# Performance work log

Measured on AMD Instinct MI355X. Metric: run time of the kernel, lower is better.

## Reference

```python
import jax, jax.numpy as jnp
import numpy as np

ALPHA = 0.2  # LeakyReLU negative slope


def setup_inputs() -> dict:
    key = jax.random.key(0)
    k1, k2, k3, k4, k5 = jax.random.split(key, 5)
    n, fin, fout = 4096, 512, 512
    X = jax.random.normal(k1, (n, fin), dtype=jnp.float32)
    # sparse-ish 0/1 adjacency with self loops so every softmax row is non-empty
    A = (jax.random.uniform(k2, (n, n)) < 0.005).astype(jnp.float32)
    A = jnp.minimum(A + jnp.eye(n, dtype=jnp.float32), 1.0)
    W_short = jax.random.normal(k3, (fout, fin), dtype=jnp.float32) * 0.02
    r = jax.random.normal(k4, (2 * fout, 1), dtype=jnp.float32) * 0.02
    W_long = jax.random.normal(k5, (fout, fin), dtype=jnp.float32) * 0.02
    return dict(X=X, A=A, W_short=W_short, r=r, W_long=W_long, num_hops=3)


def reference(X, A, W_short, r, W_long, num_hops):
    fout = W_short.shape[0]
    neg_inf = jnp.finfo(X.dtype).min

    # ---- ShortDistanceAttention ----
    Wh = X @ W_short.T                                   # (n, fout)
    # r^T [Wh_i || Wh_j] = (Wh_i . r_src) + (Wh_j . r_dst)
    src = Wh @ r[:fout, 0]                               # (n,)
    dst = Wh @ r[fout:, 0]                               # (n,)
    e = jax.nn.leaky_relu(src[:, None] + dst[None, :], ALPHA)  # (n, n)
    edge_mask = A != 0
    att = jax.nn.softmax(jnp.where(edge_mask, e, neg_inf), axis=1)
    hk = jax.nn.gelu(att @ Wh)                           # (n, fout)

    # ---- LongDistanceAttention ----
    Wa = X @ W_long.T                                    # (n, fout)
    # multi-hop reachability: union of nonzero patterns of A^1..A^num_hops
    Ak = A
    reach = A
    for _ in range(num_hops - 1):
        Ak = Ak @ A                                      # dense n^3 matmul
        reach = reach + Ak
    hop_mask = reach != 0
    scores = hk @ Wa.T                                   # (n, n)
    att2 = jax.nn.softmax(jnp.where(hop_mask, scores, neg_inf), axis=1)
    ok = att2 @ hk                                       # (n, fout)
    return ok
```

## Files before the change

### kernel.cpp

```cpp
#include <hip/hip_runtime.h>
#include <math.h>


#define N_NODES 4096
#define FDIM    512
#define MAX_NNZ 128
#define LRELU_ALPHA 0.2f
#define NUM_HOPS 3
#define PSCALE 9.765625e-4f

typedef unsigned short ushort_t;
typedef unsigned long long u64;
typedef __attribute__((ext_vector_type(8))) __bf16 bf16x8;
typedef __attribute__((ext_vector_type(8))) _Float16 f16x8;
typedef __attribute__((ext_vector_type(2))) _Float16 f16x2;
typedef __attribute__((ext_vector_type(4))) float f32x4;
typedef __attribute__((ext_vector_type(16))) float f32x16;

__device__ __forceinline__ ushort_t f2bf(float x) {
    unsigned u = __float_as_uint(x);
    u += 0x7fff + ((u >> 16) & 1);
    return (ushort_t)(u >> 16);
}
__device__ __forceinline__ float bf2f(ushort_t h) {
    return __uint_as_float((unsigned)h << 16);
}
__device__ __forceinline__ void split2(float x, ushort_t& h, ushort_t& l) {
    h = f2bf(x);
    l = f2bf(x - bf2f(h));
}
__device__ __forceinline__ ushort_t f2h(float x) {
    _Float16 v = (_Float16)x;
    return *(ushort_t*)&v;
}

__device__ __forceinline__ float gelu_tanh(float x) {
    float x3 = x * x * x;
    float t  = tanhf(0.7978845608028654f * (x + 0.044715f * x3));
    return 0.5f * x * (1.0f + t);
}

__device__ __forceinline__ void gload_lds16(const void* g, void* l) {
    __builtin_amdgcn_global_load_lds(
        (const __attribute__((address_space(1))) unsigned int*)g,
        (__attribute__((address_space(3))) unsigned int*)l, 16, 0, 0);
}

__global__ __launch_bounds__(256) void split_all(const float4* __restrict__ X,
                                                 const float4* __restrict__ Ws,
                                                 const float4* __restrict__ Wl,
                                                 ushort4* __restrict__ Xh,
                                                 ushort4* __restrict__ Xl,
                                                 ushort4* __restrict__ Wch,
                                                 ushort4* __restrict__ Wcl) {
    const int n0 = N_NODES * FDIM / 4;
    const int n1 = FDIM * FDIM / 4;
    const int total = n0 + 2 * n1;
    int i = blockIdx.x * 256 + threadIdx.x;
    int stride = gridDim.x * 256;
    for (; i < total; i += stride) {
        float4 v;
        ushort4* dh;
        ushort4* dl;
        int o;
        if (i < n0)           { v = X[i];  dh = Xh;       dl = Xl;       o = i; }
        else if (i < n0 + n1) { o = i - n0;      v = Ws[o]; dh = Wch;      dl = Wcl; }
        else                  { o = i - n0 - n1; v = Wl[o]; dh = Wch + n1; dl = Wcl + n1; }
        ushort4 h, l;
        split2(v.x, h.x, l.x); split2(v.y, h.y, l.y);
        split2(v.z, h.z, l.z); split2(v.w, h.w, l.w);
        dh[o] = h; dl[o] = l;
    }
}

__global__ __launch_bounds__(256) void transpose_f16(const ushort_t* __restrict__ src,
                                                     ushort_t* __restrict__ tf) {
    __shared__ ushort_t tile[32][33];
    int bx = blockIdx.x;
    int by = blockIdx.y;
    int tx = threadIdx.x & 31;
    int ty = threadIdx.x >> 5;
    for (int r = ty; r < 32; r += 8)
        tile[r][tx] = src[(size_t)(by * 32 + r) * FDIM + bx * 32 + tx];
    __syncthreads();
    for (int r = ty; r < 32; r += 8)
        tf[(size_t)(bx * 32 + r) * N_NODES + by * 32 + tx] = tile[tx][r];
}

__global__ __launch_bounds__(256) void gemm_score(
    const ushort_t* __restrict__ Af, int lda,
    const ushort_t* __restrict__ Bf, int ldb,
    ushort_t* __restrict__ Pout, int ldc,
    const u64* __restrict__ mask, int K) {
    constexpr int BM = 128, BN = 128;
    constexpr int WTN = BN / 2, JT = WTN / 32;

    __shared__ ushort_t As[BM * 32];
    __shared__ ushort_t Bs[BN * 32];
    __shared__ u64 mw[BM][2];

    int t = threadIdx.x;
    int wave = t >> 6, lane = t & 63;
    int wr = wave >> 1, wc = wave & 1;
    int row0 = blockIdx.y * BM, col0 = blockIdx.x * BN;

    f32x16 acc[2][JT] = {};
    int m32 = lane & 31;
    int e   = lane >> 5;

    int rr = t >> 2;
    int cs = (t & 3) ^ ((t >> 3) & 3);
    const ushort_t* pA[BM / 64];
    const ushort_t* pB[BN / 64];
#pragma unroll
    for (int q = 0; q < BM / 64; q++)
        pA[q] = Af + (size_t)(row0 + q * 64 + rr) * lda + cs * 8;
#pragma unroll
    for (int q = 0; q < BN / 64; q++)
        pB[q] = Bf + (size_t)(col0 + q * 64 + rr) * ldb + cs * 8;

    for (int ks = 0; ks < K; ks += 32) {
#pragma unroll
        for (int q = 0; q < BM / 64; q++) {
            gload_lds16(pA[q], As + (q * 256 + wave * 64) * 8);
            pA[q] += 32;
        }
#pragma unroll
        for (int q = 0; q < BN / 64; q++) {
            gload_lds16(pB[q], Bs + (q * 256 + wave * 64) * 8);
            pB[q] += 32;
        }
        __syncthreads();

        f16x8 af[2][2], bf[JT][2];
#pragma unroll
        for (int i = 0; i < 2; i++) {
            int ar = wr * 64 + i * 32 + m32;
            int sw = (ar >> 1) & 3;
#pragma unroll
            for (int kh = 0; kh < 2; kh++) {
                int slot = (kh * 2 + e) ^ sw;
                af[i][kh] = *(const f16x8*)(As + ar * 32 + slot * 8);
            }
        }
#pragma unroll
        for (int j = 0; j < JT; j++) {
            int bc = wc * WTN + j * 32 + m32;
            int sw = (bc >> 1) & 3;
#pragma unroll
            for (int kh = 0; kh < 2; kh++) {
                int slot = (kh * 2 + e) ^ sw;
                bf[j][kh] = *(const f16x8*)(Bs + bc * 32 + slot * 8);
            }
        }
#pragma unroll
        for (int i = 0; i < 2; i++)
#pragma unroll
            for (int j = 0; j < JT; j++)
#pragma unroll
                for (int kh = 0; kh < 2; kh++)
                    acc[i][j] = __builtin_amdgcn_mfma_f32_32x32x16_f16(af[i][kh], bf[j][kh], acc[i][j], 0, 0, 0);
        __syncthreads();
    }

    if (t < 2 * BM) {
        int r2 = t >> 1, w2 = t & 1;
        mw[r2][w2] = mask[(size_t)(row0 + r2) * 64 + (col0 >> 6) + w2];
    }
    __syncthreads();

    int rbase = 4 * e;
#pragma unroll
    for (int i = 0; i < 2; i++)
#pragma unroll
        for (int j = 0; j < JT; j++) {
            int cl = wc * WTN + j * 32 + m32;
            int col = col0 + cl;
#pragma unroll
            for (int rg = 0; rg < 16; rg++) {
                int rl = wr * 64 + i * 32 + (rg & 3) + 8 * (rg >> 2) + rbase;
                bool on = (mw[rl][cl >> 6] >> (cl & 63)) & 1ULL;
                float pv = on ? __expf(acc[i][j][rg]) * PSCALE : 0.0f;
                Pout[(size_t)(row0 + rl) * ldc + col] = f2h(pv);
            }
        }
}

__global__ __launch_bounds__(256) void gemm_pv(
    const ushort_t* __restrict__ Pf, int lda,
    const ushort_t* __restrict__ Bf, int ldb,
    float* __restrict__ Cf, int ldc,
    float* __restrict__ lsum, int M, int Klen) {
    constexpr int BM = 128, BN = 64;
    constexpr int WTN = BN / 2, JT = WTN / 32;

    __shared__ ushort_t As[BM * 32];
    __shared__ ushort_t Bs[BN * 32];

    int bid = blockIdx.x;
    int r8 = bid & 7;
    int g  = bid >> 3;
    int bx = g & 7;
    int yz = (g >> 3) * 8 + r8;
    int by = yz & 31, bz = yz >> 5;

    int t = threadIdx.x;
    int wave = t >> 6, lane = t & 63;
    int wr = wave >> 1, wc = wave & 1;
    int row0 = by * BM, col0 = bx * BN;
    int kb = bz * Klen;
    Cf += (size_t)bz * M * ldc;

    f32x16 acc[2][JT] = {};
    float rs[2] = {0.0f, 0.0f};
    int m32 = lane & 31;
    int e   = lane >> 5;

    int rr = t >> 2;
    int cs = (t & 3) ^ ((t >> 3) & 3);
    const ushort_t* pA[BM / 64];
#pragma unroll
    for (int q = 0; q < BM / 64; q++)
        pA[q] = Pf + (size_t)(row0 + q * 64 + rr) * lda + kb + cs * 8;
    const ushort_t* pB = Bf + (size_t)(col0 + rr) * ldb + kb + cs * 8;

    for (int ks = 0; ks < Klen; ks += 32) {
#pragma unroll
        for (int q = 0; q < BM / 64; q++) {
            gload_lds16(pA[q], As + (q * 256 + wave * 64) * 8);
            pA[q] += 32;
        }
        if (wave < 1) {
        }
        gload_lds16(pB, Bs + (wave * 64) * 8);
        pB += 32;
        __syncthreads();

        f16x8 af[2][2], bf[JT][2];
#pragma unroll
        for (int i = 0; i < 2; i++) {
            int ar = wr * 64 + i * 32 + m32;
            int sw = (ar >> 1) & 3;
#pragma unroll
            for (int kh = 0; kh < 2; kh++) {
                int slot = (kh * 2 + e) ^ sw;
                f16x8 raw = *(const f16x8*)(As + ar * 32 + slot * 8);
                af[i][kh] = raw;
                if (wc == 0) {
#pragma unroll
                    for (int k = 0; k < 8; k++) rs[i] += (float)raw[k];
                }
            }
        }
#pragma unroll
        for (int j = 0; j < JT; j++) {
            int bc = wc * WTN + j * 32 + m32;
            int sw = (bc >> 1) & 3;
#pragma unroll
            for (int kh = 0; kh < 2; kh++) {
                int slot = (kh * 2 + e) ^ sw;
                bf[j][kh] = *(const f16x8*)(Bs + bc * 32 + slot * 8);
            }
        }
#pragma unroll
        for (int i = 0; i < 2; i++)
#pragma unroll
            for (int j = 0; j < JT; j++)
#pragma unroll
                for (int kh = 0; kh < 2; kh++)
                    acc[i][j] = __builtin_amdgcn_mfma_f32_32x32x16_f16(af[i][kh], bf[j][kh], acc[i][j], 0, 0, 0);
        __syncthreads();
    }

    if (wc == 0) {
        rs[0] += __shfl_xor(rs[0], 32, 64);
        rs[1] += __shfl_xor(rs[1], 32, 64);
        if (bx == 0 && e == 0) {
            atomicAdd(&lsum[row0 + wr * 64 + m32], rs[0]);
            atomicAdd(&lsum[row0 + wr * 64 + 32 + m32], rs[1]);
        }
    }

    int rbase = 4 * e;
#pragma unroll
    for (int i = 0; i < 2; i++)
#pragma unroll
        for (int j = 0; j < JT; j++) {
            int col = col0 + wc * WTN + j * 32 + m32;
#pragma unroll
            for (int rg = 0; rg < 16; rg++) {
                int row = row0 + wr * 64 + i * 32 + (rg & 3) + 8 * (rg >> 2) + rbase;
                Cf[(size_t)row * ldc + col] = acc[i][j][rg];
            }
        }
}

template <int BM, int BN>
__global__ __launch_bounds__(256) void gemm3_nt(
    const ushort_t* __restrict__ Ah, const ushort_t* __restrict__ Al, int lda,
    const ushort_t* __restrict__ Bh, const ushort_t* __restrict__ Bl, int ldb,
    float* __restrict__ Cf, int ldc, int Klen,
    ushort_t* __restrict__ Whf, ushort_t* __restrict__ Ef) {
    constexpr int WTN = BN / 2;
    constexpr int JT  = WTN / 32;

    __shared__ ushort_t As_h[BM * 32], As_l[BM * 32];
    __shared__ ushort_t Bs_h[BN * 32], Bs_l[BN * 32];

    int t = threadIdx.x;
    int wave = t >> 6, lane = t & 63;
    int wr = wave >> 1, wc = wave & 1;
    int row0 = blockIdx.y * BM, col0 = blockIdx.x * BN;

    f32x16 acc[2][JT] = {};
    int m32 = lane & 31;
    int e   = lane >> 5;

    int rr = t >> 2;
    int cs = (t & 3) ^ ((t >> 3) & 3);
    const ushort_t* pAh[BM / 64];
    const ushort_t* pAl[BM / 64];
    const ushort_t* pBh[BN / 64];
    const ushort_t* pBl[BN / 64];
#pragma unroll
    for (int q = 0; q < BM / 64; q++) {
        size_t o = (size_t)(row0 + q * 64 + rr) * lda + cs * 8;
        pAh[q] = Ah + o; pAl[q] = Al + o;
    }
#pragma unroll
    for (int q = 0; q < BN / 64; q++) {
        size_t o = (size_t)(col0 + q * 64 + rr) * ldb + cs * 8;
        pBh[q] = Bh + o; pBl[q] = Bl + o;
    }

    for (int ks = 0; ks < Klen; ks += 32) {
#pragma unroll
        for (int q = 0; q < BM / 64; q++) {
            int ldsoff = (q * 256 + wave * 64) * 8;
            gload_lds16(pAh[q], As_h + ldsoff);
            gload_lds16(pAl[q], As_l + ldsoff);
            pAh[q] += 32; pAl[q] += 32;
        }
#pragma unroll
        for (int q = 0; q < BN / 64; q++) {
            int ldsoff = (q * 256 + wave * 64) * 8;
            gload_lds16(pBh[q], Bs_h + ldsoff);
            gload_lds16(pBl[q], Bs_l + ldsoff);
            pBh[q] += 32; pBl[q] += 32;
        }
        __syncthreads();

        bf16x8 afh[2][2], afl[2][2], bfh[JT][2], bfl[JT][2];
#pragma unroll
        for (int i = 0; i < 2; i++) {
            int ar = wr * 64 + i * 32 + m32;
            int sw = (ar >> 1) & 3;
#pragma unroll
            for (int kh = 0; kh < 2; kh++) {
                int slot = (kh * 2 + e) ^ sw;
                afh[i][kh] = *(const bf16x8*)(As_h + ar * 32 + slot * 8);
                afl[i][kh] = *(const bf16x8*)(As_l + ar * 32 + slot * 8);
            }
        }
#pragma unroll
        for (int j = 0; j < JT; j++) {
            int bc = wc * WTN + j * 32 + m32;
            int sw = (bc >> 1) & 3;
#pragma unroll
            for (int kh = 0; kh < 2; kh++) {
                int slot = (kh * 2 + e) ^ sw;
                bfh[j][kh] = *(const bf16x8*)(Bs_h + bc * 32 + slot * 8);
                bfl[j][kh] = *(const bf16x8*)(Bs_l + bc * 32 + slot * 8);
            }
        }
#pragma unroll
        for (int i = 0; i < 2; i++)
#pragma unroll
            for (int j = 0; j < JT; j++)
#pragma unroll
                for (int kh = 0; kh < 2; kh++) {
                    acc[i][j] = __builtin_amdgcn_mfma_f32_32x32x16_bf16(afh[i][kh], bfh[j][kh], acc[i][j], 0, 0, 0);
                    acc[i][j] = __builtin_amdgcn_mfma_f32_32x32x16_bf16(afh[i][kh], bfl[j][kh], acc[i][j], 0, 0, 0);
                    acc[i][j] = __builtin_amdgcn_mfma_f32_32x32x16_bf16(afl[i][kh], bfh[j][kh], acc[i][j], 0, 0, 0);
                }
        __syncthreads();
    }

    int rbase = 4 * e;
#pragma unroll
    for (int i = 0; i < 2; i++)
#pragma unroll
        for (int j = 0; j < JT; j++) {
            int col = col0 + wc * WTN + j * 32 + m32;
#pragma unroll
            for (int rg = 0; rg < 16; rg++) {
                int row = row0 + wr * 64 + i * 32 + (rg & 3) + 8 * (rg >> 2) + rbase;
                float v = acc[i][j][rg];
                if (col < FDIM) {
                    Cf[(size_t)row * ldc + col] = v;
                    Whf[(size_t)row * FDIM + col] = f2h(v);
                } else {
                    Ef[(size_t)row * FDIM + col - FDIM] = f2h(v);
                }
            }
        }
}

__global__ __launch_bounds__(256) void reduce4(const f32x4* __restrict__ P,
                                               const float* __restrict__ lsum,
                                               f32x4* __restrict__ out) {
    const size_t stride = (size_t)N_NODES * FDIM / 4;
    int i = blockIdx.x * 256 + threadIdx.x;
    f32x4 s = P[i] + P[i + stride] + P[i + 2 * stride] + P[i + 3 * stride];
    float inv = 1.0f / lsum[i >> 7];
    out[i] = s * inv;
}

__global__ __launch_bounds__(256) void srcdst_kernel(const float* __restrict__ Wh,
                                                     const float* __restrict__ r,
                                                     float* __restrict__ src,
                                                     float* __restrict__ dst) {
    int i = blockIdx.x, t = threadIdx.x;
    float ps = 0.0f, pd = 0.0f;
    for (int k = t; k < FDIM; k += 256) {
        float w = Wh[(size_t)i * FDIM + k];
        ps += w * r[k];
        pd += w * r[FDIM + k];
    }
    __shared__ float sbuf[512];
    sbuf[t] = ps; sbuf[256 + t] = pd;
    __syncthreads();
    for (int s = 128; s > 0; s >>= 1) {
        if (t < s) { sbuf[t] += sbuf[t + s]; sbuf[256 + t] += sbuf[256 + t + s]; }
        __syncthreads();
    }
    if (t == 0) { src[i] = sbuf[0]; dst[i] = sbuf[256]; }
}

__global__ __launch_bounds__(256) void prep_A(const float* __restrict__ A,
                                              int* __restrict__ nnz,
                                              int* __restrict__ idx,
                                              u64* __restrict__ bits,
                                              u64* __restrict__ reach) {
    int i = blockIdx.x, t = threadIdx.x;
    int wave = t >> 6, lane = t & 63;
    __shared__ int cnt;
    if (t == 0) cnt = 0;
    __syncthreads();
    for (int w = wave; w < 64; w += 4) {
        float a = A[(size_t)i * N_NODES + w * 64 + lane];
        bool nz = a != 0.0f;
        u64 m = __ballot(nz);
        if (lane == 0) { bits[i * 64 + w] = m; reach[i * 64 + w] = m; }
        if (nz) {
            int s = atomicAdd(&cnt, 1);
            if (s < MAX_NNZ) idx[i * MAX_NNZ + s] = w * 64 + lane;
        }
    }
    __syncthreads();
    if (t == 0) nnz[i] = cnt < MAX_NNZ ? cnt : MAX_NNZ;
}

__global__ __launch_bounds__(256) void hop_kernel(const u64* __restrict__ in,
                                                  u64* __restrict__ out,
                                                  u64* __restrict__ reach,
                                                  const int* __restrict__ nnz,
                                                  const int* __restrict__ idx) {
    int i = blockIdx.x * 4 + (threadIdx.x >> 6);
    int w = threadIdx.x & 63;
    int cnt = nnz[i];
    u64 acc = 0ULL;
    for (int q = 0; q < cnt; q++) {
        int j = idx[i * MAX_NNZ + q];
        acc |= in[(size_t)j * 64 + w];
    }
    out[i * 64 + w] = acc;
    reach[i * 64 + w] |= acc;
}

__global__ __launch_bounds__(256) void short_attn(const ushort_t* __restrict__ Whf,
                                                  const float* __restrict__ src,
                                                  const float* __restrict__ dst,
                                                  const int* __restrict__ nnz,
                                                  const int* __restrict__ idx,
                                                  ushort_t* __restrict__ hkf) {
    int i = blockIdx.x, t = threadIdx.x;
    __shared__ int   s_idx[MAX_NNZ];
    __shared__ float s_w[MAX_NNZ];
    __shared__ float s_m, s_sum;
    int cnt = nnz[i];
    float si = src[i];
    if (t < cnt) {
        int j = idx[i * MAX_NNZ + t];
        s_idx[t] = j;
        float e = si + dst[j];
        s_w[t] = e > 0.0f ? e : LRELU_ALPHA * e;
    }
    __syncthreads();
    if (t == 0) {
        float m = -INFINITY;
        for (int q = 0; q < cnt; q++) m = fmaxf(m, s_w[q]);
        s_m = m;
    }
    __syncthreads();
    if (t < cnt) s_w[t] = __expf(s_w[t] - s_m);
    __syncthreads();
    if (t == 0) {
        float s = 0.0f;
        for (int q = 0; q < cnt; q++) s += s_w[q];
        s_sum = s;
    }
    __syncthreads();
    float inv = 1.0f / s_sum;
    const f16x2* W2 = (const f16x2*)Whf;
    float ax = 0.0f, ay = 0.0f;
    for (int q = 0; q < cnt; q++) {
        float w = s_w[q];
        f16x2 v = W2[(size_t)s_idx[q] * (FDIM / 2) + t];
        ax += w * (float)v.x; ay += w * (float)v.y;
    }
    float vx = gelu_tanh(ax * inv);
    float vy = gelu_tanh(ay * inv);
    size_t o = (size_t)i * FDIM + 2 * t;
    hkf[o] = f2h(vx); hkf[o + 1] = f2h(vy);
}

extern "C" void kernel_launch(void* const* d_in, const int* in_sizes, int n_in,
                              void* d_out, int out_size, void* d_ws, size_t ws_size,
                              hipStream_t stream) {
    (void)in_sizes; (void)n_in; (void)out_size; (void)ws_size;
    const float* X       = (const float*)d_in[0];
    const float* A       = (const float*)d_in[1];
    const float* W_short = (const float*)d_in[2];
    const float* r       = (const float*)d_in[3];
    const float* W_long  = (const float*)d_in[4];

    char* p = (char*)d_ws;
    ushort_t* scoresF = (ushort_t*)p; p += (size_t)N_NODES * N_NODES * 2;
    float* Psplit = (float*)p;   p += (size_t)4 * N_NODES * FDIM * 4;
    float* Wh     = (float*)p;   p += (size_t)N_NODES * FDIM * 4;
    ushort_t* Whf = (ushort_t*)p; p += (size_t)N_NODES * FDIM * 2;
    ushort_t* Xh  = (ushort_t*)p; p += (size_t)N_NODES * FDIM * 2;
    ushort_t* Xl  = (ushort_t*)p; p += (size_t)N_NODES * FDIM * 2;
    ushort_t* Waf = (ushort_t*)p; p += (size_t)N_NODES * FDIM * 2;
    ushort_t* Wch = (ushort_t*)p; p += (size_t)1024 * FDIM * 2;
    ushort_t* Wcl = (ushort_t*)p; p += (size_t)1024 * FDIM * 2;
    int* idx      = (int*)p;     p += (size_t)N_NODES * MAX_NNZ * 4;
    u64* Abits    = (u64*)p;     p += (size_t)N_NODES * 64 * 8;
    u64* Bcur     = (u64*)p;     p += (size_t)N_NODES * 64 * 8;
    u64* Bnxt     = (u64*)p;     p += (size_t)N_NODES * 64 * 8;
    u64* reach    = (u64*)p;     p += (size_t)N_NODES * 64 * 8;
    float* lsum   = (float*)p;   p += N_NODES * 4;
    float* src    = (float*)p;   p += N_NODES * 4;
    float* dst    = (float*)p;   p += N_NODES * 4;
    int* nnz      = (int*)p;     p += N_NODES * 4;

    ushort_t* hkf  = Xh;
    ushort_t* hkTf = (ushort_t*)Wh;

    hipMemsetAsync(lsum, 0, N_NODES * 4, stream);

    split_all<<<1280, 256, 0, stream>>>((const float4*)X, (const float4*)W_short,
                                        (const float4*)W_long,
                                        (ushort4*)Xh, (ushort4*)Xl,
                                        (ushort4*)Wch, (ushort4*)Wcl);

    gemm3_nt<128, 64><<<dim3(1024 / 64, N_NODES / 128), 256, 0, stream>>>(
        Xh, Xl, FDIM, Wch, Wcl, FDIM, Wh, FDIM, FDIM, Whf, Waf);

    srcdst_kernel<<<N_NODES, 256, 0, stream>>>(Wh, r, src, dst);

    prep_A<<<N_NODES, 256, 0, stream>>>(A, nnz, idx, Abits, reach);
    const u64* in_b = Abits;
    u64* out_b = Bcur;
    for (int h = 0; h < NUM_HOPS - 1; h++) {
        hop_kernel<<<N_NODES / 4, 256, 0, stream>>>(in_b, out_b, reach, nnz, idx);
        in_b = out_b;
        out_b = (out_b == Bcur) ? Bnxt : Bcur;
    }

    short_attn<<<N_NODES, 256, 0, stream>>>(Whf, src, dst, nnz, idx, hkf);

    transpose_f16<<<dim3(FDIM / 32, N_NODES / 32), 256, 0, stream>>>(hkf, hkTf);

    gemm_score<<<dim3(N_NODES / 128, N_NODES / 128), 256, 0, stream>>>(
        hkf, FDIM, Waf, FDIM, scoresF, N_NODES, reach, FDIM);

    gemm_pv<<<1024, 256, 0, stream>>>(
        scoresF, N_NODES, hkTf, N_NODES, Psplit, FDIM, lsum, N_NODES, N_NODES / 4);

    reduce4<<<2048, 256, 0, stream>>>((const f32x4*)Psplit, lsum, (f32x4*)d_out);
}
```

Measured before the change: 282.3 us.

## Halve gemm_score row tile and add grouped block swizzle

The score GEMM tile shrinks from 128x128 to 64x128. Each wave now holds one 32-row fragment instead of two, which doubles the grid to 2048 blocks. A 1D block index with an 8-row grouping swizzle replaces the 2D grid, meant to improve L2 reuse of the B operand across neighbouring blocks. The intent is better occupancy and load balance from fewer accumulators and more blocks, at the cost of lower arithmetic intensity per block. An empty leftover branch in gemm_pv is also removed.

```diff
diff --git a/kernel.cpp b/kernel.cpp
--- a/kernel.cpp
+++ b/kernel.cpp
@@ -92,39 +92,39 @@
     const ushort_t* __restrict__ Bf, int ldb,
     ushort_t* __restrict__ Pout, int ldc,
     const u64* __restrict__ mask, int K) {
-    constexpr int BM = 128, BN = 128;
+    constexpr int BM = 64, BN = 128;
     constexpr int WTN = BN / 2, JT = WTN / 32;
 
     __shared__ ushort_t As[BM * 32];
     __shared__ ushort_t Bs[BN * 32];
     __shared__ u64 mw[BM][2];
 
+    int bid = blockIdx.x;
+    int r8 = bid & 7;
+    int g  = bid >> 3;
+    int bxt = g & 31;
+    int byt = (g >> 5) * 8 + r8;
+
     int t = threadIdx.x;
     int wave = t >> 6, lane = t & 63;
     int wr = wave >> 1, wc = wave & 1;
-    int row0 = blockIdx.y * BM, col0 = blockIdx.x * BN;
-
-    f32x16 acc[2][JT] = {};
+    int row0 = byt * BM, col0 = bxt * BN;
+
+    f32x16 acc[JT] = {};
     int m32 = lane & 31;
     int e   = lane >> 5;
 
     int rr = t >> 2;
     int cs = (t & 3) ^ ((t >> 3) & 3);
-    const ushort_t* pA[BM / 64];
+    const ushort_t* pA = Af + (size_t)(row0 + rr) * lda + cs * 8;
     const ushort_t* pB[BN / 64];
-#pragma unroll
-    for (int q = 0; q < BM / 64; q++)
-        pA[q] = Af + (size_t)(row0 + q * 64 + rr) * lda + cs * 8;
 #pragma unroll
     for (int q = 0; q < BN / 64; q++)
         pB[q] = Bf + (size_t)(col0 + q * 64 + rr) * ldb + cs * 8;
 
     for (int ks = 0; ks < K; ks += 32) {
-#pragma unroll
-        for (int q = 0; q < BM / 64; q++) {
-            gload_lds16(pA[q], As + (q * 256 + wave * 64) * 8);
-            pA[q] += 32;
-        }
+        gload_lds16(pA, As + (wave * 64) * 8);
+        pA += 32;
 #pragma unroll
         for (int q = 0; q < BN / 64; q++) {
             gload_lds16(pB[q], Bs + (q * 256 + wave * 64) * 8);
@@ -132,15 +132,14 @@
         }
         __syncthreads();
 
-        f16x8 af[2][2], bf[JT][2];
-#pragma unroll
-        for (int i = 0; i < 2; i++) {
-            int ar = wr * 64 + i * 32 + m32;
+        f16x8 af[2], bf[JT][2];
+        {
+            int ar = wr * 32 + m32;
             int sw = (ar >> 1) & 3;
 #pragma unroll
             for (int kh = 0; kh < 2; kh++) {
                 int slot = (kh * 2 + e) ^ sw;
-                af[i][kh] = *(const f16x8*)(As + ar * 32 + slot * 8);
+                af[kh] = *(const f16x8*)(As + ar * 32 + slot * 8);
             }
         }
 #pragma unroll
@@ -154,12 +153,10 @@
             }
         }
 #pragma unroll
-        for (int i = 0; i < 2; i++)
-#pragma unroll
-            for (int j = 0; j < JT; j++)
-#pragma unroll
-                for (int kh = 0; kh < 2; kh++)
-                    acc[i][j] = __builtin_amdgcn_mfma_f32_32x32x16_f16(af[i][kh], bf[j][kh], acc[i][j], 0, 0, 0);
+        for (int j = 0; j < JT; j++)
+#pragma unroll
+            for (int kh = 0; kh < 2; kh++)
+                acc[j] = __builtin_amdgcn_mfma_f32_32x32x16_f16(af[kh], bf[j][kh], acc[j], 0, 0, 0);
         __syncthreads();
     }
 
@@ -171,19 +168,17 @@
 
     int rbase = 4 * e;
 #pragma unroll
-    for (int i = 0; i < 2; i++)
-#pragma unroll
-        for (int j = 0; j < JT; j++) {
-            int cl = wc * WTN + j * 32 + m32;
-            int col = col0 + cl;
-#pragma unroll
-            for (int rg = 0; rg < 16; rg++) {
-                int rl = wr * 64 + i * 32 + (rg & 3) + 8 * (rg >> 2) + rbase;
-                bool on = (mw[rl][cl >> 6] >> (cl & 63)) & 1ULL;
-                float pv = on ? __expf(acc[i][j][rg]) * PSCALE : 0.0f;
-                Pout[(size_t)(row0 + rl) * ldc + col] = f2h(pv);
-            }
-        }
+    for (int j = 0; j < JT; j++) {
+        int cl = wc * WTN + j * 32 + m32;
+        int col = col0 + cl;
+#pragma unroll
+        for (int rg = 0; rg < 16; rg++) {
+            int rl = wr * 32 + (rg & 3) + 8 * (rg >> 2) + rbase;
+            bool on = (mw[rl][cl >> 6] >> (cl & 63)) & 1ULL;
+            float pv = on ? __expf(acc[j][rg]) * PSCALE : 0.0f;
+            Pout[(size_t)(row0 + rl) * ldc + col] = f2h(pv);
+        }
+    }
 }
 
 __global__ __launch_bounds__(256) void gemm_pv(
@@ -229,8 +224,6 @@
         for (int q = 0; q < BM / 64; q++) {
             gload_lds16(pA[q], As + (q * 256 + wave * 64) * 8);
             pA[q] += 32;
-        }
-        if (wave < 1) {
         }
         gload_lds16(pB, Bs + (wave * 64) * 8);
         pB += 32;
@@ -583,7 +576,7 @@
 
     transpose_f16<<<dim3(FDIM / 32, N_NODES / 32), 256, 0, stream>>>(hkf, hkTf);
 
-    gemm_score<<<dim3(N_NODES / 128, N_NODES / 128), 256, 0, stream>>>(
+    gemm_score<<<2048, 256, 0, stream>>>(
         hkf, FDIM, Waf, FDIM, scoresF, N_NODES, reach, FDIM);
 
     gemm_pv<<<1024, 256, 0, stream>>>(
```

Measured after the change: 284.1 us. No clear change (+0.6%).
